# Kernel optimization log

Measured on AMD Instinct MI355X. Metric: run time of the kernel, lower is better.

## Reference

```python
import jax, jax.numpy as jnp
import numpy as np

B, L, U, G, H = 64, 110, 768, 512, 256
WP = WF = 10
NSP = 2
R = 2 * NSP * NSP      # 8 relation types
NB = 30                # RGCN num_bases
FF = 2048              # torch TransformerEncoderLayer default dim_feedforward
TAG = 7
N = B * L
NEG = -1e9


def _build_edges():
    # static windowed edge structure (all dialogues have length L)
    js, ks = [], []
    for j in range(L):
        for k in range(max(0, j - WP), min(L - 1, j + WF) + 1):
            js.append(j); ks.append(k)
    j = np.asarray(js, np.int32); k = np.asarray(ks, np.int32)
    c = (j >= k).astype(np.int32)  # edge_type suffix: '0' if j<k else '1'
    off = (np.arange(B, dtype=np.int32) * L)[:, None]
    src = (j[None, :] + off).reshape(-1)
    dst = (k[None, :] + off).reshape(-1)
    return src, dst, np.tile(k, B), np.tile(c, B)


def _ln(x, g, b):
    m = x.mean(-1, keepdims=True)
    v = ((x - m) ** 2).mean(-1, keepdims=True)
    return (x - m) / jnp.sqrt(v + 1e-5) * g + b


def _core(x, in_proj_w, in_proj_b, out_proj_w, out_proj_b, ln1_g, ln1_b,
          ff1_w, ff1_b, ff2_w, ff2_b, ln2_g, ln2_b, to_w, to_b, att_w,
          rgcn_basis, rgcn_comp, rgcn_root, rgcn_bias,
          gc_rel_w, gc_rel_b, gc_root_w, clf1_w, clf1_b, clf2_w, clf2_b,
          speaker, src, dst, k_local, cflag):
    # --- SeqContext: 1-layer, 1-head post-norm transformer (eval mode) ---
    qkv = x @ in_proj_w.T + in_proj_b
    q, kk, v = jnp.split(qkv, 3, axis=-1)
    attn = jax.nn.softmax(jnp.einsum('bqd,bkd->bqk', q, kk) / jnp.sqrt(jnp.float32(U)), -1)
    a = jnp.einsum('bqk,bkd->bqd', attn, v) @ out_proj_w.T + out_proj_b
    h = _ln(x + a, ln1_g, ln1_b)
    ff = jax.nn.relu(h @ ff1_w.T + ff1_b) @ ff2_w.T + ff2_b
    h = _ln(h + ff, ln2_g, ln2_b)
    feats = h @ to_w.T + to_b                      # (B, L, G) node features

    # --- EdgeAtt: windowed softmax attention, score[j,k] = x_j^T W x_k ---
    scores = jnp.einsum('bjd,de,bke->bjk', feats, att_w, feats)
    rel = jnp.arange(L)[None, :] - jnp.arange(L)[:, None]
    mask = (rel >= -WP) & (rel <= WF)
    alpha = jax.nn.softmax(jnp.where(mask[None], scores, NEG), -1)  # (B, L, L)

    xf = feats.reshape(N, G)
    edge_norm = alpha.reshape(N, L)[src, k_local]   # alpha[b, j, k] per edge

    # --- edge types from speakers: idx = (s1*NSP + s2)*2 + c ---
    sp = speaker.reshape(N)
    etype = (sp[src] * NSP + sp[dst]) * 2 + cflag

    # --- RGCNConv: basis decomposition, per-(node, relation) mean + root ---
    w_rel = jnp.einsum('rb,bgh->rgh', rgcn_comp, rgcn_basis)   # (R, G, H)
    xproj = jnp.einsum('ng,rgh->rnh', xf, w_rel)               # (R, N, H)
    msg = xproj[etype, src]                                    # (E, H)
    seg = dst * R + etype
    cnt = jax.ops.segment_sum(jnp.ones_like(edge_norm), seg, num_segments=N * R)
    msg = msg / jnp.maximum(cnt[seg], 1.0)[:, None]
    h1 = jax.ops.segment_sum(msg, dst, num_segments=N) + xf @ rgcn_root + rgcn_bias

    # --- GraphConv: sum-aggregate edge-weighted neighbors + root ---
    agg = jax.ops.segment_sum(edge_norm[:, None] * h1[src], dst, num_segments=N)
    h2 = agg @ gc_rel_w.T + gc_rel_b + h1 @ gc_root_w.T

    # --- Classifier (dropout inactive in eval) ---
    z = jnp.concatenate([xf, h2], axis=-1)
    return jax.nn.relu(z @ clf1_w.T + clf1_b) @ clf2_w.T + clf2_b  # (N, TAG)


def setup_inputs():
    key = jax.random.key(0)
    ks = jax.random.split(key, 16)
    def rn(i, shape, scale=0.02):
        return jax.random.normal(ks[i], shape, jnp.float32) * scale
    src, dst, k_local, cflag = _build_edges()
    return {
        'x': jax.random.normal(ks[0], (B, L, U), jnp.float32),
        'in_proj_w': rn(1, (3 * U, U)), 'in_proj_b': jnp.zeros((3 * U,), jnp.float32),
        'out_proj_w': rn(2, (U, U)), 'out_proj_b': jnp.zeros((U,), jnp.float32),
        'ln1_g': jnp.ones((U,), jnp.float32), 'ln1_b': jnp.zeros((U,), jnp.float32),
        'ff1_w': rn(3, (FF, U)), 'ff1_b': jnp.zeros((FF,), jnp.float32),
        'ff2_w': rn(4, (U, FF)), 'ff2_b': jnp.zeros((U,), jnp.float32),
        'ln2_g': jnp.ones((U,), jnp.float32), 'ln2_b': jnp.zeros((U,), jnp.float32),
        'to_w': rn(5, (G, U)), 'to_b': jnp.zeros((G,), jnp.float32),
        'att_w': rn(6, (G, G), 2.0 / (G + G)),
        'rgcn_basis': rn(7, (NB, G, H)), 'rgcn_comp': rn(8, (R, NB), 0.2),
        'rgcn_root': rn(9, (G, H)), 'rgcn_bias': jnp.zeros((H,), jnp.float32),
        'gc_rel_w': rn(10, (H, H)), 'gc_rel_b': jnp.zeros((H,), jnp.float32),
        'gc_root_w': rn(11, (H, H)),
        'clf1_w': rn(12, (H, G + H)), 'clf1_b': jnp.zeros((H,), jnp.float32),
        'clf2_w': rn(13, (TAG, H)), 'clf2_b': jnp.zeros((TAG,), jnp.float32),
        'speaker': jax.random.randint(ks[14], (B, L), 0, NSP, jnp.int32),
        'src': jnp.asarray(src), 'dst': jnp.asarray(dst),
        'k_local': jnp.asarray(k_local), 'cflag': jnp.asarray(cflag),
        'length': L,
    }


def reference(x, in_proj_w, in_proj_b, out_proj_w, out_proj_b, ln1_g, ln1_b,
              ff1_w, ff1_b, ff2_w, ff2_b, ln2_g, ln2_b, to_w, to_b, att_w,
              rgcn_basis, rgcn_comp, rgcn_root, rgcn_bias,
              gc_rel_w, gc_rel_b, gc_root_w, clf1_w, clf1_b, clf2_w, clf2_b,
              speaker, src, dst, k_local, cflag, length):
    return _core(x, in_proj_w, in_proj_b, out_proj_w, out_proj_b, ln1_g, ln1_b,
                 ff1_w, ff1_b, ff2_w, ff2_b, ln2_g, ln2_b, to_w, to_b, att_w,
                 rgcn_basis, rgcn_comp, rgcn_root, rgcn_bias,
                 gc_rel_w, gc_rel_b, gc_root_w, clf1_w, clf1_b, clf2_w, clf2_b,
                 speaker, src, dst, k_local, cflag)
```

## Files before the change

kernel.cpp:

```cpp
#include <hip/hip_runtime.h>
#include <hip/hip_bf16.h>
#include <math.h>

#define L_   110
#define B_   64
#define N_   7040
#define U_   768
#define G_   512
#define H_   256
#define FF_  2048
#define EPB_ 2200
#define NC_  2816

typedef __attribute__((ext_vector_type(4))) float f32x4;
typedef __attribute__((ext_vector_type(8))) short bf16x8;

__device__ __forceinline__ ushort f2b(float f) {
  union { __hip_bfloat16 h; ushort u; } cv;
  cv.h = __float2bfloat16(f);
  return cv.u;
}
__device__ __forceinline__ float b2f(ushort u) {
  union { float f; unsigned int i; } cv; cv.i = ((unsigned int)u) << 16; return cv.f;
}

__device__ __forceinline__ int edge_prefix(int j) {
  if (j <= 10)  return j * 11 + (j * (j - 1)) / 2;
  if (j <= 100) return 155 + (j - 10) * 21;
  return 2045 + ((141 - j) * (j - 100)) / 2;
}

struct Segs7 { const float* in[7]; ushort* out[7]; int n4[7]; };

__global__ __launch_bounds__(256)
void cvtmulti_kernel(Segs7 s)
{
  const int seg = blockIdx.y;
  const int n4 = s.n4[seg];
  const float* __restrict__ in = s.in[seg];
  ushort* __restrict__ out = s.out[seg];
  for (int i = blockIdx.x * 256 + threadIdx.x; i < n4; i += gridDim.x * 256) {
    float4 v = ((const float4*)in)[i];
    ushort4 o;
    o.x = f2b(v.x); o.y = f2b(v.y); o.z = f2b(v.z); o.w = f2b(v.w);
    ((ushort4*)out)[i] = o;
  }
}

__global__ __launch_bounds__(256)
void tcvt_kernel(const float* __restrict__ in, ushort* __restrict__ out,
                 int R, int C, size_t inStride, size_t outStride)
{
  __shared__ float t[32][33];
  const int bt = blockIdx.z;
  const int r0 = blockIdx.y * 32, c0 = blockIdx.x * 32;
  const int tx = threadIdx.x & 31, ty = threadIdx.x >> 5;
  for (int i = ty; i < 32; i += 8)
    t[i][tx] = in[bt * inStride + (size_t)(r0 + i) * C + c0 + tx];
  __syncthreads();
  for (int i = ty; i < 32; i += 8)
    out[bt * outStride + (size_t)(c0 + i) * R + r0 + tx] = f2b(t[tx][i]);
}

__global__ __launch_bounds__(256)
void wrel_kernel(const float* __restrict__ basis, const float* __restrict__ comp,
                 float* __restrict__ wrel)
{
  __shared__ float cs[240];
  const int tid = threadIdx.x;
  if (tid < 240) cs[tid] = comp[tid];
  __syncthreads();
  const int gh = blockIdx.x * 256 + tid;
  float acc[8] = {};
  for (int bb = 0; bb < 30; ++bb) {
    float v = basis[(size_t)bb * (G_ * H_) + gh];
#pragma unroll
    for (int r = 0; r < 8; ++r) acc[r] = fmaf(cs[r * 30 + bb], v, acc[r]);
  }
#pragma unroll
  for (int r = 0; r < 8; ++r) wrel[(size_t)r * (G_ * H_) + gh] = acc[r];
}

__global__ __launch_bounds__(256)
void prepmisc_kernel(const float* __restrict__ rb, const float* __restrict__ rel,
                     const float* __restrict__ root, float* __restrict__ bias,
                     ushort* __restrict__ gccat, ushort* __restrict__ vt)
{
  const int i = blockIdx.x * 256 + threadIdx.x;
  if (i < NC_) {
    bias[i] = (i < 2560) ? 0.f : rb[i - 2560];
  } else if (i < NC_ + 65536) {
    const int j = i - NC_;
    const int r = j >> 8, c = j & 255;
    gccat[(size_t)r * 512 + c]       = f2b(rel[j]);
    gccat[(size_t)r * 512 + 256 + c] = f2b(root[j]);
  } else if (i < NC_ + 65536 + 64 * 768 * 18) {
    const int j = i - (NC_ + 65536);
    const int bd = j / 18, kk = 110 + (j - bd * 18);
    vt[(size_t)bd * 128 + kk] = 0;
  }
}

template<bool BIAS, bool RELU, bool OUTB, bool VTOUT>
__global__ __launch_bounds__(256)
void mgemm_kernel(const ushort* __restrict__ A, const ushort* __restrict__ B,
                  const float* __restrict__ bias, ushort* __restrict__ Cb,
                  ushort* __restrict__ Vt,
                  int K, int lda, int ldb, int ldc)
{
  __shared__ ushort sA[128 * 64];
  __shared__ ushort sB[128 * 64];
  const int tid = threadIdx.x;
  const int w = tid >> 6, l = tid & 63;

  const int gx = gridDim.x;
  const int nwg = gx * gridDim.y;
  const int lid = blockIdx.y * gx + blockIdx.x;
  const int q = nwg >> 3, r = nwg & 7;
  const int xcd = lid & 7, pos = lid >> 3;
  const int nlid = (xcd < r ? xcd * (q + 1) : r * (q + 1) + (xcd - r) * q) + pos;
  const int m0 = (nlid / gx) * 128, n0 = (nlid % gx) * 128;

  const int srow = l >> 3, sg = l & 7, rbase = w * 32;
  const int wr = w >> 1, wc = w & 1;
  const int lrow = l & 15, lk = l >> 4;
  const int xm = (l & 7) << 4;
  const int kb0 = (lk * 16) ^ xm;
  int aoff[4], boff[4];
#pragma unroll
  for (int i = 0; i < 4; ++i) {
    aoff[i] = (wr * 64 + i * 16 + lrow) * 128 + kb0;
    boff[i] = (wc * 64 + i * 16 + lrow) * 128 + kb0;
  }

  f32x4 acc[4][4];
#pragma unroll
  for (int i = 0; i < 4; ++i)
#pragma unroll
    for (int j = 0; j < 4; ++j) acc[i][j] = (f32x4){0.f, 0.f, 0.f, 0.f};

#define STAGE(k0)                                                              \
  {                                                                            \
    _Pragma("unroll")                                                          \
    for (int i = 0; i < 4; ++i) {                                              \
      const int trow = rbase + i * 8 + srow;                                   \
      const int koff = (sg * 8) ^ ((trow & 7) << 3);                           \
      const ushort* ga = A + (size_t)(m0 + trow) * lda + (k0) + koff;          \
      const ushort* gb = B + (size_t)(n0 + trow) * ldb + (k0) + koff;          \
      __builtin_amdgcn_global_load_lds(                                        \
          (const __attribute__((address_space(1))) void*)ga,                   \
          (__attribute__((address_space(3))) void*)&sA[(rbase + i * 8) * 64],  \
          16, 0, 0);                                                           \
      __builtin_amdgcn_global_load_lds(                                        \
          (const __attribute__((address_space(1))) void*)gb,                   \
          (__attribute__((address_space(3))) void*)&sB[(rbase + i * 8) * 64],  \
          16, 0, 0);                                                           \
    }                                                                          \
  }

  STAGE(0)
  for (int kt = 0;;) {
    __syncthreads();
#pragma unroll
    for (int h = 0; h < 2; ++h) {
      const int hx = h * 64;
      bf16x8 af[4], bfr[4];
#pragma unroll
      for (int i = 0; i < 4; ++i) {
        af[i]  = *(const bf16x8*)&sA[(aoff[i] ^ hx) >> 1];
        bfr[i] = *(const bf16x8*)&sB[(boff[i] ^ hx) >> 1];
      }
#pragma unroll
      for (int mi = 0; mi < 4; ++mi)
#pragma unroll
        for (int ni = 0; ni < 4; ++ni)
          acc[mi][ni] = __builtin_amdgcn_mfma_f32_16x16x32_bf16(
              af[mi], bfr[ni], acc[mi][ni], 0, 0, 0);
    }
    kt += 64;
    if (kt >= K) break;
    __syncthreads();
    STAGE(kt)
  }
#undef STAGE

  const int orow = m0 + wr * 64 + lk * 4;
  const int ocol = n0 + wc * 64 + lrow;
#pragma unroll
  for (int mi = 0; mi < 4; ++mi) {
#pragma unroll
    for (int r2 = 0; r2 < 4; ++r2) {
      const int row = orow + mi * 16 + r2;
#pragma unroll
      for (int ni = 0; ni < 4; ++ni) {
        const int col = ocol + ni * 16;
        float v = acc[mi][ni][r2];
        if constexpr (BIAS) v += bias[col];
        if constexpr (RELU) v = fmaxf(v, 0.f);
        const ushort vb = f2b(v);
        if constexpr (OUTB) Cb[(size_t)row * ldc + col] = vb;
        if constexpr (VTOUT) {
          if (col >= 1536) {
            const int brow = row / L_, kk = row - brow * L_;
            Vt[((size_t)brow * 768 + (col - 1536)) * 128 + kk] = vb;
          }
        }
      }
    }
  }
}

__global__ __launch_bounds__(256)
void attnM_kernel(const ushort* __restrict__ qkvb, const ushort* __restrict__ vt,
                  ushort* __restrict__ ctxb)
{
  const int wg = blockIdx.x;
  const int xcd = wg & 7, slot = wg >> 3;
  const int b = xcd * 8 + slot / 7;
  const int qr0 = (slot % 7) * 16;
  const int tid = threadIdx.x, w = tid >> 6, l = tid & 63;
  __shared__ float  sS[16 * 128];
  __shared__ ushort sP[16 * 128];
  const int lrow = l & 15, lq = l >> 4;

  const ushort* Qbase = qkvb + ((size_t)(b * L_) + qr0 + lrow) * 2304 + lq * 8;
  f32x4 accS[2] = {{0.f,0.f,0.f,0.f},{0.f,0.f,0.f,0.f}};
  const int nf0 = w * 2;
  for (int k0 = 0; k0 < 768; k0 += 32) {
    bf16x8 aq = *(const bf16x8*)(Qbase + k0);
#pragma unroll
    for (int f = 0; f < 2; ++f) {
      const int nf = nf0 + f;
      if (nf < 7) {
        const ushort* Kp = qkvb + ((size_t)(b * L_) + nf * 16 + lrow) * 2304
                         + 768 + k0 + lq * 8;
        bf16x8 bk = *(const bf16x8*)Kp;
        accS[f] = __builtin_amdgcn_mfma_f32_16x16x32_bf16(aq, bk, accS[f], 0, 0, 0);
      }
    }
  }
  const float scale = 0.03608439182435161f;
#pragma unroll
  for (int f = 0; f < 2; ++f) {
    const int nf = nf0 + f;
    if (nf < 7) {
#pragma unroll
      for (int r = 0; r < 4; ++r)
        sS[(lq * 4 + r) * 128 + nf * 16 + lrow] = accS[f][r] * scale;
    }
  }
  __syncthreads();

  {
    const int row = w * 4 + lq;
    const int c0 = lrow;
    float m = -1e30f;
    for (int c = c0; c < L_; c += 16) m = fmaxf(m, sS[row * 128 + c]);
#pragma unroll
    for (int off = 8; off; off >>= 1) m = fmaxf(m, __shfl_xor(m, off));
    float pv[7];
    float sum = 0.f;
#pragma unroll
    for (int i = 0; i < 7; ++i) {
      const int c = c0 + i * 16;
      float e = (c < L_) ? __expf(sS[row * 128 + c] - m) : 0.f;
      pv[i] = e; sum += e;
    }
#pragma unroll
    for (int off = 8; off; off >>= 1) sum += __shfl_xor(sum, off);
    const float inv = 1.f / sum;
#pragma unroll
    for (int i = 0; i < 8; ++i) {
      const int c = c0 + i * 16;
      ushort pb = (i < 7 && c < L_) ? f2b(pv[i < 7 ? i : 0] * inv) : (ushort)0;
      const int g = (c >> 3) ^ (row & 7);
      sP[row * 128 + g * 8 + (c & 7)] = pb;
    }
  }
  __syncthreads();

  f32x4 accO[12];
#pragma unroll
  for (int i = 0; i < 12; ++i) accO[i] = (f32x4){0.f, 0.f, 0.f, 0.f};
#pragma unroll
  for (int ks = 0; ks < 4; ++ks) {
    const int k = ks * 32 + lq * 8;
    const int g = (k >> 3) ^ (lrow & 7);
    bf16x8 ap = *(const bf16x8*)&sP[lrow * 128 + g * 8];
#pragma unroll
    for (int i = 0; i < 12; ++i) {
      const int col = w * 192 + i * 16 + lrow;
      bf16x8 bv = *(const bf16x8*)(vt + ((size_t)b * 768 + col) * 128 + k);
      accO[i] = __builtin_amdgcn_mfma_f32_16x16x32_bf16(ap, bv, accO[i], 0, 0, 0);
    }
  }
#pragma unroll
  for (int i = 0; i < 12; ++i) {
    const int col = w * 192 + i * 16 + lrow;
#pragma unroll
    for (int r = 0; r < 4; ++r) {
      const int row = qr0 + lq * 4 + r;
      if (row < L_)
        ctxb[((size_t)b * L_ + row) * 768 + col] = f2b(accO[i][r]);
    }
  }
}

template<bool WF>
__global__ __launch_bounds__(256)
void ln_kernel(const float* __restrict__ A, const ushort* __restrict__ Bres,
               const float* __restrict__ g, const float* __restrict__ beta,
               float* __restrict__ out, ushort* __restrict__ outb)
{
  const int row = blockIdx.x, tid = threadIdx.x;
  const float* ap = A + (size_t)row * U_;
  const ushort* bp = Bres + (size_t)row * U_;
  float v0 = ap[tid] + b2f(bp[tid]);
  float v1 = ap[tid + 256] + b2f(bp[tid + 256]);
  float v2 = ap[tid + 512] + b2f(bp[tid + 512]);
  float s = v0 + v1 + v2, sq = v0 * v0 + v1 * v1 + v2 * v2;
  __shared__ float red[8];
#pragma unroll
  for (int off = 32; off; off >>= 1) { s += __shfl_xor(s, off); sq += __shfl_xor(sq, off); }
  const int wave = tid >> 6, lane = tid & 63;
  if (lane == 0) { red[wave] = s; red[4 + wave] = sq; }
  __syncthreads();
  if (tid == 0) {
    float ts = red[0] + red[1] + red[2] + red[3];
    float tq = red[4] + red[5] + red[6] + red[7];
    float m = ts * (1.f / 768.f);
    float var = tq * (1.f / 768.f) - m * m;
    red[0] = m; red[1] = 1.f / sqrtf(var + 1e-5f);
  }
  __syncthreads();
  const float m = red[0], inv = red[1];
  ushort* ob = outb + (size_t)row * U_;
  float o0 = (v0 - m) * inv * g[tid] + beta[tid];
  float o1 = (v1 - m) * inv * g[tid + 256] + beta[tid + 256];
  float o2 = (v2 - m) * inv * g[tid + 512] + beta[tid + 512];
  if constexpr (WF) {
    float* op = out + (size_t)row * U_;
    op[tid] = o0; op[tid + 256] = o1; op[tid + 512] = o2;
  }
  ob[tid] = f2b(o0); ob[tid + 256] = f2b(o1); ob[tid + 512] = f2b(o2);
}

__global__ __launch_bounds__(256)
void graphfront_kernel(const ushort* __restrict__ combo, const ushort* __restrict__ fcat,
                       const int* __restrict__ speaker,
                       ushort* __restrict__ catb, float* __restrict__ edge_norm)
{
  const int tid = threadIdx.x;
  if (blockIdx.x < N_ / 8) {
    const int n = blockIdx.x * 8 + (tid >> 5);
    const int lane = tid & 31;
    const int b = n / L_, k = n - b * L_;
    const int j0 = max(0, k - 10), j1 = min(L_ - 1, k + 10);
    const int spk = speaker[n];
    float inv[4];
    {
      int cn[4] = {0, 0, 0, 0};
      for (int j = j0; j <= j1; ++j)
        cn[speaker[b * L_ + j] * 2 + (j >= k ? 1 : 0)]++;
#pragma unroll
      for (int q = 0; q < 4; ++q) inv[q] = cn[q] ? 1.f / (float)cn[q] : 0.f;
    }
    float acc[8] = {};
    for (int j = j0; j <= j1; ++j) {
      const int spj = speaker[b * L_ + j];
      const int c = (j >= k) ? 1 : 0;
      const int et = (spj * 2 + spk) * 2 + c;
      const float w = inv[spj * 2 + c];
      bf16x8 v = *(const bf16x8*)&combo[(size_t)(b * L_ + j) * NC_ + 512 + et * 256 + lane * 8];
#pragma unroll
      for (int i = 0; i < 8; ++i) acc[i] = fmaf(b2f((ushort)v[i]), w, acc[i]);
    }
    bf16x8 rt = *(const bf16x8*)&combo[(size_t)n * NC_ + 2560 + lane * 8];
    bf16x8 o;
#pragma unroll
    for (int i = 0; i < 8; ++i) o[i] = (short)f2b(acc[i] + b2f((ushort)rt[i]));
    *(bf16x8*)&catb[(size_t)n * 512 + 256 + lane * 8] = o;
  } else {
    const int bj = blockIdx.x - N_ / 8;
    const int b = bj / L_, j = bj - b * L_;
    const int k0 = max(0, j - 10), k1 = min(L_ - 1, j + 10);
    __shared__ float s[32];
    const int wave = tid >> 6, lane = tid & 63;
    float tr[8];
    {
      bf16x8 tv = *(const bf16x8*)&combo[(size_t)bj * NC_ + lane * 8];
#pragma unroll
      for (int i = 0; i < 8; ++i) tr[i] = b2f((ushort)tv[i]);
    }
    for (int k = k0 + wave; k <= k1; k += 4) {
      bf16x8 v = *(const bf16x8*)&fcat[(size_t)(b * L_ + k) * 768 + lane * 8];
      float sc = 0.f;
#pragma unroll
      for (int i = 0; i < 8; ++i) sc = fmaf(b2f((ushort)v[i]), tr[i], sc);
#pragma unroll
      for (int off = 32; off; off >>= 1) sc += __shfl_xor(sc, off);
      if (lane == 0) s[k - k0] = sc;
    }
    __syncthreads();
    if (tid == 0) {
      const int W = k1 - k0 + 1;
      float m = -1e30f;
      for (int t = 0; t < W; ++t) m = fmaxf(m, s[t]);
      float sum = 0.f;
      for (int t = 0; t < W; ++t) { float e = __expf(s[t] - m); s[t] = e; sum += e; }
      const float inv = 1.f / sum;
      const int base = b * EPB_ + edge_prefix(j);
      for (int t = 0; t < W; ++t) edge_norm[base + t] = s[t] * inv;
    }
  }
}

__global__ __launch_bounds__(256)
void gcn_gather2_kernel(const float* __restrict__ edge_norm,
                        ushort* __restrict__ catb)
{
  const int tid = threadIdx.x;
  const int n = blockIdx.x * 8 + (tid >> 5);
  const int lane = tid & 31;
  const int b = n / L_, k = n - b * L_;
  const int j0 = max(0, k - 10), j1 = min(L_ - 1, k + 10);
  float acc[8] = {};
  for (int j = j0; j <= j1; ++j) {
    const float w = edge_norm[b * EPB_ + edge_prefix(j) + (k - max(0, j - 10))];
    bf16x8 v = *(const bf16x8*)&catb[(size_t)(b * L_ + j) * 512 + 256 + lane * 8];
#pragma unroll
    for (int i = 0; i < 8; ++i) acc[i] = fmaf(b2f((ushort)v[i]), w, acc[i]);
  }
  bf16x8 o;
#pragma unroll
  for (int i = 0; i < 8; ++i) o[i] = (short)f2b(acc[i]);
  *(bf16x8*)&catb[(size_t)n * 512 + lane * 8] = o;
}

__global__ __launch_bounds__(256)
void clf2_kernel(const ushort* __restrict__ hid, const float* __restrict__ w,
                 const float* __restrict__ bias, float* __restrict__ out)
{
  __shared__ float wsm[7 * H_];
  const int tid = threadIdx.x;
  for (int i = tid; i < 7 * H_; i += 256) wsm[i] = w[i];
  __syncthreads();
  const int idx = blockIdx.x * 256 + threadIdx.x;
  if (idx < N_ * 7) {
    const int n = idx / 7, t = idx - n * 7;
    const ushort* hp = hid + (size_t)n * H_;
    const float* wp = wsm + t * H_;
    float acc = bias[t];
    for (int d0 = 0; d0 < H_; d0 += 8) {
      bf16x8 v = *(const bf16x8*)(hp + d0);
#pragma unroll
      for (int i = 0; i < 8; ++i) acc = fmaf(b2f((ushort)v[i]), wp[d0 + i], acc);
    }
    out[idx] = acc;
  }
}

extern "C" void kernel_launch(void* const* d_in, const int* in_sizes, int n_in,
                              void* d_out, int out_size, void* d_ws, size_t ws_size,
                              hipStream_t stream)
{
  const float* x          = (const float*)d_in[0];
  const float* in_proj_w  = (const float*)d_in[1];
  const float* in_proj_b  = (const float*)d_in[2];
  const float* out_proj_w = (const float*)d_in[3];
  const float* out_proj_b = (const float*)d_in[4];
  const float* ln1_g      = (const float*)d_in[5];
  const float* ln1_b      = (const float*)d_in[6];
  const float* ff1_w      = (const float*)d_in[7];
  const float* ff1_b      = (const float*)d_in[8];
  const float* ff2_w      = (const float*)d_in[9];
  const float* ff2_b      = (const float*)d_in[10];
  const float* ln2_g      = (const float*)d_in[11];
  const float* ln2_b      = (const float*)d_in[12];
  const float* to_w       = (const float*)d_in[13];
  const float* to_b       = (const float*)d_in[14];
  const float* att_w      = (const float*)d_in[15];
  const float* rgcn_basis = (const float*)d_in[16];
  const float* rgcn_comp  = (const float*)d_in[17];
  const float* rgcn_root  = (const float*)d_in[18];
  const float* rgcn_bias  = (const float*)d_in[19];
  const float* gc_rel_w   = (const float*)d_in[20];
  const float* gc_rel_b   = (const float*)d_in[21];
  const float* gc_root_w  = (const float*)d_in[22];
  const float* clf1_w     = (const float*)d_in[23];
  const float* clf1_b     = (const float*)d_in[24];
  const float* clf2_w     = (const float*)d_in[25];
  const float* clf2_b     = (const float*)d_in[26];
  const int*   speaker    = (const int*)d_in[27];
  float* out = (float*)d_out;
  char* p = (char*)d_ws;

  float*  R1f    = (float*)p;
  ushort* R1b    = (ushort*)p;
  p += (size_t)N_ * 2304 * 4;
  ushort* aprojB = (ushort*)p;
  ushort* ffoB   = aprojB;
  float*  en     = (float*)(p + (size_t)N_ * 512 * 4);
  p += (size_t)N_ * 768 * 4;
  float*  hbuf  = (float*)p;
  ushort* vt    = (ushort*)p;
  ushort* hidB  = (ushort*)p;
  p += (size_t)N_ * 768 * 4;
  ushort* xb    = (ushort*)p;
  ushort* ctxb  = xb;
  p += (size_t)N_ * 768 * 2;
  ushort* hb    = (ushort*)p;
  ushort* catb  = hb;
  p += (size_t)N_ * 768 * 2;
  ushort* fcat  = (ushort*)p; p += (size_t)N_ * 768 * 2;
  ushort* in_projb = (ushort*)p; p += (size_t)2304 * 768 * 2;
  ushort* out_projb= (ushort*)p; p += (size_t)768 * 768 * 2;
  ushort* ff1b     = (ushort*)p; p += (size_t)2048 * 768 * 2;
  ushort* ff2b     = (ushort*)p; p += (size_t)768 * 2048 * 2;
  ushort* tob      = (ushort*)p; p += (size_t)512 * 768 * 2;
  ushort* combw    = (ushort*)p; p += (size_t)NC_ * 512 * 2;
  ushort* gccat    = (ushort*)p; p += (size_t)256 * 512 * 2;
  ushort* clf1b16  = (ushort*)p; p += (size_t)256 * 768 * 2;
  float*  bias_comb= (float*)p;  p += NC_ * 4;
  float*  wrelTmp  = R1f;

  Segs7 segs;
  segs.in[0] = x;          segs.out[0] = xb;        segs.n4[0] = N_ * 768 / 4;
  segs.in[1] = in_proj_w;  segs.out[1] = in_projb;  segs.n4[1] = 2304 * 768 / 4;
  segs.in[2] = out_proj_w; segs.out[2] = out_projb; segs.n4[2] = 768 * 768 / 4;
  segs.in[3] = ff1_w;      segs.out[3] = ff1b;      segs.n4[3] = 2048 * 768 / 4;
  segs.in[4] = ff2_w;      segs.out[4] = ff2b;      segs.n4[4] = 768 * 2048 / 4;
  segs.in[5] = to_w;       segs.out[5] = tob;       segs.n4[5] = 512 * 768 / 4;
  segs.in[6] = clf1_w;     segs.out[6] = clf1b16;   segs.n4[6] = 256 * 768 / 4;
  cvtmulti_kernel<<<dim3(768, 7), 256, 0, stream>>>(segs);
  prepmisc_kernel<<<(NC_ + 65536 + 64 * 768 * 18 + 255) / 256, 256, 0, stream>>>(
      rgcn_bias, gc_rel_w, gc_root_w, bias_comb, gccat, vt);
  tcvt_kernel<<<dim3(16, 16, 1), 256, 0, stream>>>(att_w, combw, 512, 512, 0, 0);
  wrel_kernel<<<512, 256, 0, stream>>>(rgcn_basis, rgcn_comp, wrelTmp);
  tcvt_kernel<<<dim3(8, 16, 8), 256, 0, stream>>>(wrelTmp, combw + (size_t)512 * 512,
                                                  512, 256,
                                                  (size_t)512 * 256, (size_t)256 * 512);
  tcvt_kernel<<<dim3(8, 16, 1), 256, 0, stream>>>(rgcn_root, combw + (size_t)2560 * 512,
                                                  512, 256, 0, 0);

  mgemm_kernel<true, false, true, true><<<dim3(18, 55), 256, 0, stream>>>(
      xb, in_projb, in_proj_b, R1b, vt, 768, 768, 768, 2304);
  attnM_kernel<<<448, 256, 0, stream>>>(R1b, vt, ctxb);
  mgemm_kernel<true, false, true, false><<<dim3(6, 55), 256, 0, stream>>>(
      ctxb, out_projb, out_proj_b, aprojB, nullptr, 768, 768, 768, 768);
  ln_kernel<true><<<N_, 256, 0, stream>>>(x, aprojB, ln1_g, ln1_b, hbuf, hb);
  mgemm_kernel<true, true, true, false><<<dim3(16, 55), 256, 0, stream>>>(
      hb, ff1b, ff1_b, R1b, nullptr, 768, 768, 768, 2048);
  mgemm_kernel<true, false, true, false><<<dim3(6, 55), 256, 0, stream>>>(
      R1b, ff2b, ff2_b, ffoB, nullptr, 2048, 2048, 2048, 768);
  ln_kernel<false><<<N_, 256, 0, stream>>>(hbuf, ffoB, ln2_g, ln2_b, nullptr, hb);
  mgemm_kernel<true, false, true, false><<<dim3(4, 55), 256, 0, stream>>>(
      hb, tob, to_b, fcat, nullptr, 768, 768, 768, 768);
  mgemm_kernel<true, false, true, false><<<dim3(22, 55), 256, 0, stream>>>(
      fcat, combw, bias_comb, R1b, nullptr, 512, 768, 512, NC_);
  graphfront_kernel<<<N_ / 8 + N_, 256, 0, stream>>>(R1b, fcat, speaker, catb, en);
  gcn_gather2_kernel<<<N_ / 8, 256, 0, stream>>>(en, catb);
  mgemm_kernel<true, false, true, false><<<dim3(2, 55), 256, 0, stream>>>(
      catb, gccat, gc_rel_b, fcat + 512, nullptr, 512, 512, 512, 768);
  mgemm_kernel<true, true, true, false><<<dim3(2, 55), 256, 0, stream>>>(
      fcat, clf1b16, clf1_b, hidB, nullptr, 768, 768, 768, 256);
  clf2_kernel<<<(N_ * 7 + 255) / 256, 256, 0, stream>>>(hidB, clf2_w, clf2_b, out);
}
```

Measured before the change: 337.1 us.

## Move V transpose to a tiled kernel and drop fp32 LayerNorm residual buffer

The scattered transposed V write is removed from the QKV GEMM epilogue and replaced by a separate shared-memory tiled transpose kernel, which also zero-fills the padding rows. This makes prepmisc's zero-pad pass unnecessary. The first LayerNorm no longer writes an fp32 copy of its output, and the second LayerNorm reads the bf16 residual instead. This trims global writes and uncoalesced stores but adds a kernel launch, and using the bf16 residual slightly lowers precision.

```diff
diff --git a/kernel.cpp b/kernel.cpp
--- a/kernel.cpp
+++ b/kernel.cpp
@@ -84,7 +84,7 @@
 __global__ __launch_bounds__(256)
 void prepmisc_kernel(const float* __restrict__ rb, const float* __restrict__ rel,
                      const float* __restrict__ root, float* __restrict__ bias,
-                     ushort* __restrict__ gccat, ushort* __restrict__ vt)
+                     ushort* __restrict__ gccat)
 {
   const int i = blockIdx.x * 256 + threadIdx.x;
   if (i < NC_) {
@@ -94,18 +94,13 @@
     const int r = j >> 8, c = j & 255;
     gccat[(size_t)r * 512 + c]       = f2b(rel[j]);
     gccat[(size_t)r * 512 + 256 + c] = f2b(root[j]);
-  } else if (i < NC_ + 65536 + 64 * 768 * 18) {
-    const int j = i - (NC_ + 65536);
-    const int bd = j / 18, kk = 110 + (j - bd * 18);
-    vt[(size_t)bd * 128 + kk] = 0;
-  }
-}
-
-template<bool BIAS, bool RELU, bool OUTB, bool VTOUT>
+  }
+}
+
+template<bool BIAS, bool RELU>
 __global__ __launch_bounds__(256)
 void mgemm_kernel(const ushort* __restrict__ A, const ushort* __restrict__ B,
                   const float* __restrict__ bias, ushort* __restrict__ Cb,
-                  ushort* __restrict__ Vt,
                   int K, int lda, int ldb, int ldc)
 {
   __shared__ ushort sA[128 * 64];
@@ -197,17 +192,28 @@
         float v = acc[mi][ni][r2];
         if constexpr (BIAS) v += bias[col];
         if constexpr (RELU) v = fmaxf(v, 0.f);
-        const ushort vb = f2b(v);
-        if constexpr (OUTB) Cb[(size_t)row * ldc + col] = vb;
-        if constexpr (VTOUT) {
-          if (col >= 1536) {
-            const int brow = row / L_, kk = row - brow * L_;
-            Vt[((size_t)brow * 768 + (col - 1536)) * 128 + kk] = vb;
-          }
-        }
+        Cb[(size_t)row * ldc + col] = f2b(v);
       }
     }
   }
+}
+
+__global__ __launch_bounds__(256)
+void vtrans_kernel(const ushort* __restrict__ qkvb, ushort* __restrict__ vt)
+{
+  __shared__ ushort t[32][33];
+  const int b = blockIdx.z;
+  const int r0 = blockIdx.y * 32;
+  const int c0 = blockIdx.x * 32;
+  const int tx = threadIdx.x & 31, ty = threadIdx.x >> 5;
+  for (int i = ty; i < 32; i += 8) {
+    const int r = r0 + i;
+    t[i][tx] = (r < L_) ? qkvb[((size_t)(b * L_) + r) * 2304 + 1536 + c0 + tx]
+                        : (ushort)0;
+  }
+  __syncthreads();
+  for (int i = ty; i < 32; i += 8)
+    vt[((size_t)b * 768 + c0 + i) * 128 + r0 + tx] = t[tx][i];
 }
 
 __global__ __launch_bounds__(256)
@@ -306,18 +312,26 @@
   }
 }
 
-template<bool WF>
-__global__ __launch_bounds__(256)
-void ln_kernel(const float* __restrict__ A, const ushort* __restrict__ Bres,
+template<bool AF32>
+__global__ __launch_bounds__(256)
+void ln_kernel(const float* __restrict__ Af, const ushort* __restrict__ Ab,
+               const ushort* __restrict__ Bres,
                const float* __restrict__ g, const float* __restrict__ beta,
-               float* __restrict__ out, ushort* __restrict__ outb)
+               ushort* __restrict__ outb)
 {
   const int row = blockIdx.x, tid = threadIdx.x;
-  const float* ap = A + (size_t)row * U_;
   const ushort* bp = Bres + (size_t)row * U_;
-  float v0 = ap[tid] + b2f(bp[tid]);
-  float v1 = ap[tid + 256] + b2f(bp[tid + 256]);
-  float v2 = ap[tid + 512] + b2f(bp[tid + 512]);
+  float a0, a1, a2;
+  if constexpr (AF32) {
+    const float* ap = Af + (size_t)row * U_;
+    a0 = ap[tid]; a1 = ap[tid + 256]; a2 = ap[tid + 512];
+  } else {
+    const ushort* ap = Ab + (size_t)row * U_;
+    a0 = b2f(ap[tid]); a1 = b2f(ap[tid + 256]); a2 = b2f(ap[tid + 512]);
+  }
+  float v0 = a0 + b2f(bp[tid]);
+  float v1 = a1 + b2f(bp[tid + 256]);
+  float v2 = a2 + b2f(bp[tid + 512]);
   float s = v0 + v1 + v2, sq = v0 * v0 + v1 * v1 + v2 * v2;
   __shared__ float red[8];
 #pragma unroll
@@ -335,14 +349,9 @@
   __syncthreads();
   const float m = red[0], inv = red[1];
   ushort* ob = outb + (size_t)row * U_;
-  float o0 = (v0 - m) * inv * g[tid] + beta[tid];
-  float o1 = (v1 - m) * inv * g[tid + 256] + beta[tid + 256];
-  float o2 = (v2 - m) * inv * g[tid + 512] + beta[tid + 512];
-  if constexpr (WF) {
-    float* op = out + (size_t)row * U_;
-    op[tid] = o0; op[tid + 256] = o1; op[tid + 512] = o2;
-  }
-  ob[tid] = f2b(o0); ob[tid + 256] = f2b(o1); ob[tid + 512] = f2b(o2);
+  ob[tid]       = f2b((v0 - m) * inv * g[tid]       + beta[tid]);
+  ob[tid + 256] = f2b((v1 - m) * inv * g[tid + 256] + beta[tid + 256]);
+  ob[tid + 512] = f2b((v2 - m) * inv * g[tid + 512] + beta[tid + 512]);
 }
 
 __global__ __launch_bounds__(256)
@@ -502,7 +511,6 @@
   ushort* ffoB   = aprojB;
   float*  en     = (float*)(p + (size_t)N_ * 512 * 4);
   p += (size_t)N_ * 768 * 4;
-  float*  hbuf  = (float*)p;
   ushort* vt    = (ushort*)p;
   ushort* hidB  = (ushort*)p;
   p += (size_t)N_ * 768 * 4;
@@ -533,8 +541,8 @@
   segs.in[5] = to_w;       segs.out[5] = tob;       segs.n4[5] = 512 * 768 / 4;
   segs.in[6] = clf1_w;     segs.out[6] = clf1b16;   segs.n4[6] = 256 * 768 / 4;
   cvtmulti_kernel<<<dim3(768, 7), 256, 0, stream>>>(segs);
-  prepmisc_kernel<<<(NC_ + 65536 + 64 * 768 * 18 + 255) / 256, 256, 0, stream>>>(
-      rgcn_bias, gc_rel_w, gc_root_w, bias_comb, gccat, vt);
+  prepmisc_kernel<<<(NC_ + 65536 + 255) / 256, 256, 0, stream>>>(
+      rgcn_bias, gc_rel_w, gc_root_w, bias_comb, gccat);
   tcvt_kernel<<<dim3(16, 16, 1), 256, 0, stream>>>(att_w, combw, 512, 512, 0, 0);
   wrel_kernel<<<512, 256, 0, stream>>>(rgcn_basis, rgcn_comp, wrelTmp);
   tcvt_kernel<<<dim3(8, 16, 8), 256, 0, stream>>>(wrelTmp, combw + (size_t)512 * 512,
@@ -543,26 +551,27 @@
   tcvt_kernel<<<dim3(8, 16, 1), 256, 0, stream>>>(rgcn_root, combw + (size_t)2560 * 512,
                                                   512, 256, 0, 0);
 
-  mgemm_kernel<true, false, true, true><<<dim3(18, 55), 256, 0, stream>>>(
-      xb, in_projb, in_proj_b, R1b, vt, 768, 768, 768, 2304);
+  mgemm_kernel<true, false><<<dim3(18, 55), 256, 0, stream>>>(
+      xb, in_projb, in_proj_b, R1b, 768, 768, 768, 2304);
+  vtrans_kernel<<<dim3(24, 4, 64), 256, 0, stream>>>(R1b, vt);
   attnM_kernel<<<448, 256, 0, stream>>>(R1b, vt, ctxb);
-  mgemm_kernel<true, false, true, false><<<dim3(6, 55), 256, 0, stream>>>(
-      ctxb, out_projb, out_proj_b, aprojB, nullptr, 768, 768, 768, 768);
-  ln_kernel<true><<<N_, 256, 0, stream>>>(x, aprojB, ln1_g, ln1_b, hbuf, hb);
-  mgemm_kernel<true, true, true, false><<<dim3(16, 55), 256, 0, stream>>>(
-      hb, ff1b, ff1_b, R1b, nullptr, 768, 768, 768, 2048);
-  mgemm_kernel<true, false, true, false><<<dim3(6, 55), 256, 0, stream>>>(
-      R1b, ff2b, ff2_b, ffoB, nullptr, 2048, 2048, 2048, 768);
-  ln_kernel<false><<<N_, 256, 0, stream>>>(hbuf, ffoB, ln2_g, ln2_b, nullptr, hb);
-  mgemm_kernel<true, false, true, false><<<dim3(4, 55), 256, 0, stream>>>(
-      hb, tob, to_b, fcat, nullptr, 768, 768, 768, 768);
-  mgemm_kernel<true, false, true, false><<<dim3(22, 55), 256, 0, stream>>>(
-      fcat, combw, bias_comb, R1b, nullptr, 512, 768, 512, NC_);
+  mgemm_kernel<true, false><<<dim3(6, 55), 256, 0, stream>>>(
+      ctxb, out_projb, out_proj_b, aprojB, 768, 768, 768, 768);
+  ln_kernel<true><<<N_, 256, 0, stream>>>(x, nullptr, aprojB, ln1_g, ln1_b, hb);
+  mgemm_kernel<true, true><<<dim3(16, 55), 256, 0, stream>>>(
+      hb, ff1b, ff1_b, R1b, 768, 768, 768, 2048);
+  mgemm_kernel<true, false><<<dim3(6, 55), 256, 0, stream>>>(
+      R1b, ff2b, ff2_b, ffoB, 2048, 2048, 2048, 768);
+  ln_kernel<false><<<N_, 256, 0, stream>>>(nullptr, hb, ffoB, ln2_g, ln2_b, hb);
+  mgemm_kernel<true, false><<<dim3(4, 55), 256, 0, stream>>>(
+      hb, tob, to_b, fcat, 768, 768, 768, 768);
+  mgemm_kernel<true, false><<<dim3(22, 55), 256, 0, stream>>>(
+      fcat, combw, bias_comb, R1b, 512, 768, 512, NC_);
   graphfront_kernel<<<N_ / 8 + N_, 256, 0, stream>>>(R1b, fcat, speaker, catb, en);
   gcn_gather2_kernel<<<N_ / 8, 256, 0, stream>>>(en, catb);
-  mgemm_kernel<true, false, true, false><<<dim3(2, 55), 256, 0, stream>>>(
-      catb, gccat, gc_rel_b, fcat + 512, nullptr, 512, 512, 512, 768);
-  mgemm_kernel<true, true, true, false><<<dim3(2, 55), 256, 0, stream>>>(
-      fcat, clf1b16, clf1_b, hidB, nullptr, 768, 768, 768, 256);
+  mgemm_kernel<true, false><<<dim3(2, 55), 256, 0, stream>>>(
+      catb, gccat, gc_rel_b, fcat + 512, 512, 512, 512, 768);
+  mgemm_kernel<true, true><<<dim3(2, 55), 256, 0, stream>>>(
+      fcat, clf1b16, clf1_b, hidB, 768, 768, 768, 256);
   clf2_kernel<<<(N_ * 7 + 255) / 256, 256, 0, stream>>>(hidB, clf2_w, clf2_b, out);
 }
```

Result: faster. 322.2 us (-4.4%).
